# Performance work log

Measured on AMD Instinct MI355X. Metric: run time of the kernel, lower is better.

Reference implementation:

```python
import jax, jax.numpy as jnp
import numpy as np

B, N, D = 256, 512, 64  # batch, positions, channels; units = spatial_units = D


def setup_inputs() -> dict:
    key = jax.random.key(0)
    ks = jax.random.split(key, 9)
    g = 1.0 / np.sqrt(D)  # glorot-ish scale for square matrices
    return {
        "x": jax.random.normal(ks[0], (B, N, D), dtype=jnp.float32),
        "Wq_t": jax.random.normal(ks[1], (D, D), dtype=jnp.float32) * g,
        "Wk_t": jax.random.normal(ks[2], (D, D), dtype=jnp.float32) * g,
        "Wv_t": jax.random.normal(ks[3], (D, D), dtype=jnp.float32) * g,
        "Wq_s": jax.random.normal(ks[4], (D, D), dtype=jnp.float32) * g,
        "Wk_s": jax.random.normal(ks[5], (D, D), dtype=jnp.float32) * g,
        "Wv_s": jax.random.normal(ks[6], (D, D), dtype=jnp.float32) * g,
        "Wd_t": jax.random.normal(ks[7], (D, D), dtype=jnp.float32) * g,
        "bd_t": jnp.zeros((D,), dtype=jnp.float32),
        "Wd_s": jax.random.normal(ks[8], (D, D), dtype=jnp.float32) * g,
        "bd_s": jnp.zeros((D,), dtype=jnp.float32),
    }


def _branch(x, Wq, Wk, Wv, Wd, bd):
    # x: [B, N, D]; one self-attention branch followed by a Dense layer.
    q = jnp.einsum("bnd,de->bne", x, Wq)
    k = jnp.einsum("bnd,de->bne", x, Wk)
    v = jnp.einsum("bnd,de->bne", x, Wv)
    scale = 1.0 / jnp.sqrt(jnp.asarray(Wk.shape[-1], dtype=x.dtype))
    scores = jnp.einsum("bne,bme->bnm", q, k) * scale  # [B, N, N]
    w = jax.nn.softmax(scores, axis=-1)
    attn = jnp.einsum("bnm,bmd->bnd", w, v)
    return jnp.einsum("bnd,de->bne", attn, Wd) + bd


def reference(x, Wq_t, Wk_t, Wv_t, Wq_s, Wk_s, Wv_s, Wd_t, bd_t, Wd_s, bd_s):
    temporal = _branch(x, Wq_t, Wk_t, Wv_t, Wd_t, bd_t)
    spatial = _branch(x, Wq_s, Wk_s, Wv_s, Wd_s, bd_s)
    gate = jax.nn.sigmoid(temporal + spatial)
    return x * gate
```

## Files before the change

### kernel.cpp

```cpp
#include <hip/hip_runtime.h>

typedef __attribute__((ext_vector_type(8))) short short8;
typedef __attribute__((ext_vector_type(4))) short short4v;
typedef __attribute__((ext_vector_type(4))) float float4v;

#define MFMA16(a, b, c) __builtin_amdgcn_mfma_f32_16x16x32_bf16((a), (b), (c), 0, 0, 0)

constexpr int kN = 512;
constexpr int kD = 64;
constexpr int kThreads = 1024;

constexpr int LDS_TOTAL_BYTES = 79872 * 2;

static __device__ __forceinline__ unsigned short f2bf(float f) {
  unsigned int u = __float_as_uint(f);
  u = (u + 0x7fffu + ((u >> 16) & 1u)) >> 16;
  return (unsigned short)u;
}

__global__ __launch_bounds__(kThreads, 4) void ts_attn_fused(
    const float* __restrict__ x, const float* __restrict__ Wq_t,
    const float* __restrict__ Wk_t, const float* __restrict__ Wv_t,
    const float* __restrict__ Wq_s, const float* __restrict__ Wk_s,
    const float* __restrict__ Wv_s, const float* __restrict__ Wd_t,
    const float* __restrict__ bd_t, const float* __restrict__ Wd_s,
    const float* __restrict__ bd_s, float* __restrict__ out,
    unsigned short* __restrict__ qws) {
  extern __shared__ __align__(16) unsigned short smem_us[];
  unsigned short* Ksw = smem_us;
  unsigned short* Vsw = smem_us + 32768;
  unsigned short* Wdsw = smem_us + 65536;
  unsigned short* rep = smem_us + 69632;

  const int tid = threadIdx.x;
  const int wv = tid >> 6;
  const int lane = tid & 63;
  const int ln = lane & 15;
  const int quad = lane >> 4;
  const int b = blockIdx.x;

  const float* xb = x + (size_t)b * (kN * kD);
  float* outb = out + (size_t)b * (kN * kD);
  unsigned short* qb = qws + (size_t)b * (kN * kD);

  const int sd = tid >> 4;
  const int se0 = (tid & 15) * 4;
  const int sbase = (sd >> 3) * 512 + (sd & 7);

  float bdsum[4];
#pragma unroll
  for (int nt = 0; nt < 4; ++nt) bdsum[nt] = bd_t[nt * 16 + ln] + bd_s[nt * 16 + ln];

  float4v acc_t[2][4];

#pragma unroll 1
  for (int br = 0; br < 2; ++br) {
    const float* Wq = br ? Wq_s : Wq_t;
    const float* Wk = br ? Wk_s : Wk_t;
    const float* Wv = br ? Wv_s : Wv_t;
    const float* Wd = br ? Wd_s : Wd_t;

    {
      const float* srcs[3] = {Wq, Wk, Wv};
      unsigned short* dsts[3] = {rep, rep + 4096, Wdsw};
#pragma unroll
      for (int g = 0; g < 3; ++g) {
        const float4v u = *reinterpret_cast<const float4v*>(srcs[g] + sd * 64 + se0);
        unsigned short* dst = dsts[g];
#pragma unroll
        for (int i = 0; i < 4; ++i) dst[sbase + (se0 + i) * 8] = f2bf(u[i]);
      }
    }
    __syncthreads();

#pragma unroll 1
    for (int mi = 0; mi < 2; ++mi) {
      const int mt = wv + mi * 16;
      const int mrow = mt * 16 + ln;
      short8 xa0, xa1;
      {
        const float4v* p0 = reinterpret_cast<const float4v*>(xb + mrow * 64 + quad * 8);
        const float4v u0 = p0[0], v0 = p0[1];
        const float4v* p1 = reinterpret_cast<const float4v*>(xb + mrow * 64 + 32 + quad * 8);
        const float4v u1 = p1[0], v1 = p1[1];
#pragma unroll
        for (int i = 0; i < 4; ++i) {
          xa0[i] = (short)f2bf(u0[i]);
          xa0[4 + i] = (short)f2bf(v0[i]);
          xa1[i] = (short)f2bf(u1[i]);
          xa1[4 + i] = (short)f2bf(v1[i]);
        }
      }
#pragma unroll
      for (int g = 0; g < 3; ++g) {
        const unsigned short* Wl = (g == 0) ? rep : (g == 1) ? (rep + 4096) : Wdsw;
#pragma unroll
        for (int nt = 0; nt < 4; ++nt) {
          const short8 b0 = *reinterpret_cast<const short8*>(Wl + quad * 512 + (nt * 16 + ln) * 8);
          const short8 b1 = *reinterpret_cast<const short8*>(Wl + (4 + quad) * 512 + (nt * 16 + ln) * 8);
          float4v acc = {0.f, 0.f, 0.f, 0.f};
          acc = MFMA16(xa0, b0, acc);
          acc = MFMA16(xa1, b1, acc);
          if (g == 0) {
            const int ehi = nt * 2 + (ln >> 3);
            const int elo = ln & 7;
#pragma unroll
            for (int r = 0; r < 4; ++r)
              qb[ehi * 4096 + (mt * 16 + quad * 4 + r) * 8 + elo] = f2bf(acc[r]);
          } else if (g == 1) {
            const int ehi = nt * 2 + (ln >> 3);
            const int elo = ln & 7;
#pragma unroll
            for (int r = 0; r < 4; ++r)
              Ksw[ehi * 4096 + (mt * 16 + quad * 4 + r) * 8 + elo] = f2bf(acc[r]);
          } else {
            short4v pk;
#pragma unroll
            for (int r = 0; r < 4; ++r) pk[r] = (short)f2bf(acc[r]);
            const int vbase =
                (mt * 2 + (quad >> 1)) * 512 + (nt * 16 + ln) * 8 + (quad & 1) * 4;
            *reinterpret_cast<short4v*>(Vsw + vbase) = pk;
          }
        }
      }
    }
    __syncthreads();

    {
      const float4v u = *reinterpret_cast<const float4v*>(Wd + sd * 64 + se0);
#pragma unroll
      for (int i = 0; i < 4; ++i) Wdsw[sbase + (se0 + i) * 8] = f2bf(u[i]);
    }
    __syncthreads();

    unsigned short* buf = rep + wv * 640;
#pragma unroll 1
    for (int qi = 0; qi < 2; ++qi) {
      const int qt = wv + qi * 16;
      const short8 q0 = *reinterpret_cast<const short8*>(qb + quad * 4096 + (qt * 16 + ln) * 8);
      const short8 q1 = *reinterpret_cast<const short8*>(qb + (4 + quad) * 4096 + (qt * 16 + ln) * 8);

      float sum[4] = {0.f, 0.f, 0.f, 0.f};
      float4v o[4];
#pragma unroll
      for (int i = 0; i < 4; ++i) o[i] = (float4v){0.f, 0.f, 0.f, 0.f};

#pragma unroll 2
      for (int kc = 0; kc < 16; ++kc) {
#pragma unroll
        for (int t2 = 0; t2 < 2; ++t2) {
          const int nt = kc * 2 + t2;
          const short8 k0 = *reinterpret_cast<const short8*>(Ksw + quad * 4096 + (nt * 16 + ln) * 8);
          const short8 k1 =
              *reinterpret_cast<const short8*>(Ksw + (4 + quad) * 4096 + (nt * 16 + ln) * 8);
          float4v acc = {0.f, 0.f, 0.f, 0.f};
          acc = MFMA16(q0, k0, acc);
          acc = MFMA16(q1, k1, acc);
#pragma unroll
          for (int r = 0; r < 4; ++r) {
            const float p = __expf(acc[r] * 0.125f);
            sum[r] += p;
            buf[(quad * 4 + r) * 40 + t2 * 16 + ln] = f2bf(p);
          }
        }
        asm volatile("s_waitcnt lgkmcnt(0)" ::: "memory");
        const short8 pa = *reinterpret_cast<const short8*>(buf + ln * 40 + quad * 8);
#pragma unroll
        for (int nto = 0; nto < 4; ++nto) {
          const short8 vf =
              *reinterpret_cast<const short8*>(Vsw + (kc * 4 + quad) * 512 + (nto * 16 + ln) * 8);
          o[nto] = MFMA16(pa, vf, o[nto]);
        }
        asm volatile("s_waitcnt lgkmcnt(0)" ::: "memory");
      }

#pragma unroll
      for (int dd = 1; dd < 16; dd <<= 1)
#pragma unroll
        for (int r = 0; r < 4; ++r) sum[r] += __shfl_xor(sum[r], dd, 64);
      float inv[4];
#pragma unroll
      for (int r = 0; r < 4; ++r) inv[r] = 1.0f / sum[r];

#pragma unroll
      for (int nto = 0; nto < 2; ++nto)
#pragma unroll
        for (int r = 0; r < 4; ++r)
          buf[(quad * 4 + r) * 40 + nto * 16 + ln] = f2bf(o[nto][r] * inv[r]);
      asm volatile("s_waitcnt lgkmcnt(0)" ::: "memory");
      const short8 a0 = *reinterpret_cast<const short8*>(buf + ln * 40 + quad * 8);
      asm volatile("s_waitcnt lgkmcnt(0)" ::: "memory");
#pragma unroll
      for (int nto = 2; nto < 4; ++nto)
#pragma unroll
        for (int r = 0; r < 4; ++r)
          buf[(quad * 4 + r) * 40 + (nto - 2) * 16 + ln] = f2bf(o[nto][r] * inv[r]);
      asm volatile("s_waitcnt lgkmcnt(0)" ::: "memory");
      const short8 a1 = *reinterpret_cast<const short8*>(buf + ln * 40 + quad * 8);

#pragma unroll
      for (int nt = 0; nt < 4; ++nt) {
        const short8 w0 = *reinterpret_cast<const short8*>(Wdsw + quad * 512 + (nt * 16 + ln) * 8);
        const short8 w1 = *reinterpret_cast<const short8*>(Wdsw + (4 + quad) * 512 + (nt * 16 + ln) * 8);
        float4v d4 = {0.f, 0.f, 0.f, 0.f};
        d4 = MFMA16(a0, w0, d4);
        d4 = MFMA16(a1, w1, d4);
        if (br == 0) {
          acc_t[qi][nt] = d4;
        } else {
          const int m0 = qt * 16 + quad * 4;
          const int col = nt * 16 + ln;
#pragma unroll
          for (int r = 0; r < 4; ++r) {
            const float z = acc_t[qi][nt][r] + d4[r] + bdsum[nt];
            const float gate = 1.0f / (1.0f + __expf(-z));
            outb[(m0 + r) * 64 + col] = xb[(m0 + r) * 64 + col] * gate;
          }
        }
      }
    }
    __syncthreads();
  }
}

extern "C" void kernel_launch(void* const* d_in, const int* in_sizes, int n_in,
                              void* d_out, int out_size, void* d_ws, size_t ws_size,
                              hipStream_t stream) {
  const float* x = (const float*)d_in[0];
  const float* Wq_t = (const float*)d_in[1];
  const float* Wk_t = (const float*)d_in[2];
  const float* Wv_t = (const float*)d_in[3];
  const float* Wq_s = (const float*)d_in[4];
  const float* Wk_s = (const float*)d_in[5];
  const float* Wv_s = (const float*)d_in[6];
  const float* Wd_t = (const float*)d_in[7];
  const float* bd_t = (const float*)d_in[8];
  const float* Wd_s = (const float*)d_in[9];
  const float* bd_s = (const float*)d_in[10];
  float* out = (float*)d_out;
  unsigned short* qws = (unsigned short*)d_ws;

  hipFuncSetAttribute(reinterpret_cast<const void*>(ts_attn_fused),
                      hipFuncAttributeMaxDynamicSharedMemorySize, LDS_TOTAL_BYTES);
  ts_attn_fused<<<dim3(256), dim3(kThreads), LDS_TOTAL_BYTES, stream>>>(
      x, Wq_t, Wk_t, Wv_t, Wq_s, Wk_s, Wv_s, Wd_t, bd_t, Wd_s, bd_s, out, qws);
}
```

Baseline: 208.7 us.

## Keep Q in registers, batch score MFMAs, spill temporal branch result to output

Q is now kept in registers and transposed through the per-wave LDS scratch buffer, so it no longer makes a round trip through a global workspace. The score loop computes eight S tiles back to back before the softmax and PV phase, which reduces the s_waitcnt stalls between MFMA groups. The temporal branch result is written to the output buffer and read back in the spatial branch, replacing the acc_t registers. This frees registers at the cost of an extra global write and read per element.

Result: no change. 205.6 us (-1.5%).

```diff
diff --git a/kernel.cpp b/kernel.cpp
--- a/kernel.cpp
+++ b/kernel.cpp
@@ -24,8 +24,7 @@
     const float* __restrict__ Wq_s, const float* __restrict__ Wk_s,
     const float* __restrict__ Wv_s, const float* __restrict__ Wd_t,
     const float* __restrict__ bd_t, const float* __restrict__ Wd_s,
-    const float* __restrict__ bd_s, float* __restrict__ out,
-    unsigned short* __restrict__ qws) {
+    const float* __restrict__ bd_s, float* __restrict__ out) {
   extern __shared__ __align__(16) unsigned short smem_us[];
   unsigned short* Ksw = smem_us;
   unsigned short* Vsw = smem_us + 32768;
@@ -41,7 +40,6 @@
 
   const float* xb = x + (size_t)b * (kN * kD);
   float* outb = out + (size_t)b * (kN * kD);
-  unsigned short* qb = qws + (size_t)b * (kN * kD);
 
   const int sd = tid >> 4;
   const int se0 = (tid & 15) * 4;
@@ -50,8 +48,6 @@
   float bdsum[4];
 #pragma unroll
   for (int nt = 0; nt < 4; ++nt) bdsum[nt] = bd_t[nt * 16 + ln] + bd_s[nt * 16 + ln];
-
-  float4v acc_t[2][4];
 
 #pragma unroll 1
   for (int br = 0; br < 2; ++br) {
@@ -73,6 +69,7 @@
     }
     __syncthreads();
 
+    short4v qd[2][4];
 #pragma unroll 1
     for (int mi = 0; mi < 2; ++mi) {
       const int mt = wv + mi * 16;
@@ -97,16 +94,16 @@
 #pragma unroll
         for (int nt = 0; nt < 4; ++nt) {
           const short8 b0 = *reinterpret_cast<const short8*>(Wl + quad * 512 + (nt * 16 + ln) * 8);
-          const short8 b1 = *reinterpret_cast<const short8*>(Wl + (4 + quad) * 512 + (nt * 16 + ln) * 8);
+          const short8 b1 =
+              *reinterpret_cast<const short8*>(Wl + (4 + quad) * 512 + (nt * 16 + ln) * 8);
           float4v acc = {0.f, 0.f, 0.f, 0.f};
           acc = MFMA16(xa0, b0, acc);
           acc = MFMA16(xa1, b1, acc);
           if (g == 0) {
-            const int ehi = nt * 2 + (ln >> 3);
-            const int elo = ln & 7;
-#pragma unroll
-            for (int r = 0; r < 4; ++r)
-              qb[ehi * 4096 + (mt * 16 + quad * 4 + r) * 8 + elo] = f2bf(acc[r]);
+            short4v pk;
+#pragma unroll
+            for (int r = 0; r < 4; ++r) pk[r] = (short)f2bf(acc[r]);
+            qd[mi][nt] = pk;
           } else if (g == 1) {
             const int ehi = nt * 2 + (ln >> 3);
             const int elo = ln & 7;
@@ -117,8 +114,7 @@
             short4v pk;
 #pragma unroll
             for (int r = 0; r < 4; ++r) pk[r] = (short)f2bf(acc[r]);
-            const int vbase =
-                (mt * 2 + (quad >> 1)) * 512 + (nt * 16 + ln) * 8 + (quad & 1) * 4;
+            const int vbase = (mt * 2 + (quad >> 1)) * 512 + (nt * 16 + ln) * 8 + (quad & 1) * 4;
             *reinterpret_cast<short4v*>(Vsw + vbase) = pk;
           }
         }
@@ -137,41 +133,65 @@
 #pragma unroll 1
     for (int qi = 0; qi < 2; ++qi) {
       const int qt = wv + qi * 16;
-      const short8 q0 = *reinterpret_cast<const short8*>(qb + quad * 4096 + (qt * 16 + ln) * 8);
-      const short8 q1 = *reinterpret_cast<const short8*>(qb + (4 + quad) * 4096 + (qt * 16 + ln) * 8);
+
+      short8 q0, q1;
+#pragma unroll
+      for (int nt = 0; nt < 2; ++nt)
+#pragma unroll
+        for (int r = 0; r < 4; ++r)
+          buf[(quad * 4 + r) * 40 + nt * 16 + ln] = (unsigned short)qd[qi][nt][r];
+      asm volatile("s_waitcnt lgkmcnt(0)" ::: "memory");
+      q0 = *reinterpret_cast<const short8*>(buf + ln * 40 + quad * 8);
+#pragma unroll
+      for (int nt = 2; nt < 4; ++nt)
+#pragma unroll
+        for (int r = 0; r < 4; ++r)
+          buf[(quad * 4 + r) * 40 + (nt - 2) * 16 + ln] = (unsigned short)qd[qi][nt][r];
+      asm volatile("s_waitcnt lgkmcnt(0)" ::: "memory");
+      q1 = *reinterpret_cast<const short8*>(buf + ln * 40 + quad * 8);
 
       float sum[4] = {0.f, 0.f, 0.f, 0.f};
       float4v o[4];
 #pragma unroll
       for (int i = 0; i < 4; ++i) o[i] = (float4v){0.f, 0.f, 0.f, 0.f};
 
-#pragma unroll 2
-      for (int kc = 0; kc < 16; ++kc) {
-#pragma unroll
-        for (int t2 = 0; t2 < 2; ++t2) {
-          const int nt = kc * 2 + t2;
-          const short8 k0 = *reinterpret_cast<const short8*>(Ksw + quad * 4096 + (nt * 16 + ln) * 8);
+#pragma unroll 1
+      for (int sc = 0; sc < 4; ++sc) {
+        float4v s[8];
+#pragma unroll
+        for (int t = 0; t < 8; ++t) {
+          const int nt = sc * 8 + t;
+          const short8 k0 =
+              *reinterpret_cast<const short8*>(Ksw + quad * 4096 + (nt * 16 + ln) * 8);
           const short8 k1 =
               *reinterpret_cast<const short8*>(Ksw + (4 + quad) * 4096 + (nt * 16 + ln) * 8);
           float4v acc = {0.f, 0.f, 0.f, 0.f};
           acc = MFMA16(q0, k0, acc);
           acc = MFMA16(q1, k1, acc);
-#pragma unroll
-          for (int r = 0; r < 4; ++r) {
-            const float p = __expf(acc[r] * 0.125f);
-            sum[r] += p;
-            buf[(quad * 4 + r) * 40 + t2 * 16 + ln] = f2bf(p);
-          }
-        }
-        asm volatile("s_waitcnt lgkmcnt(0)" ::: "memory");
-        const short8 pa = *reinterpret_cast<const short8*>(buf + ln * 40 + quad * 8);
-#pragma unroll
-        for (int nto = 0; nto < 4; ++nto) {
-          const short8 vf =
-              *reinterpret_cast<const short8*>(Vsw + (kc * 4 + quad) * 512 + (nto * 16 + ln) * 8);
-          o[nto] = MFMA16(pa, vf, o[nto]);
-        }
-        asm volatile("s_waitcnt lgkmcnt(0)" ::: "memory");
+          s[t] = acc;
+        }
+#pragma unroll
+        for (int kc2 = 0; kc2 < 4; ++kc2) {
+          const int kcg = sc * 4 + kc2;
+#pragma unroll
+          for (int t2 = 0; t2 < 2; ++t2) {
+            const float4v sv = s[kc2 * 2 + t2];
+#pragma unroll
+            for (int r = 0; r < 4; ++r) {
+              const float p = __expf(sv[r] * 0.125f);
+              sum[r] += p;
+              buf[(quad * 4 + r) * 40 + t2 * 16 + ln] = f2bf(p);
+            }
+          }
+          asm volatile("s_waitcnt lgkmcnt(0)" ::: "memory");
+          const short8 pa = *reinterpret_cast<const short8*>(buf + ln * 40 + quad * 8);
+#pragma unroll
+          for (int nto = 0; nto < 4; ++nto) {
+            const short8 vf =
+                *reinterpret_cast<const short8*>(Vsw + (kcg * 4 + quad) * 512 + (nto * 16 + ln) * 8);
+            o[nto] = MFMA16(pa, vf, o[nto]);
+          }
+        }
       }
 
 #pragma unroll
@@ -189,7 +209,6 @@
           buf[(quad * 4 + r) * 40 + nto * 16 + ln] = f2bf(o[nto][r] * inv[r]);
       asm volatile("s_waitcnt lgkmcnt(0)" ::: "memory");
       const short8 a0 = *reinterpret_cast<const short8*>(buf + ln * 40 + quad * 8);
-      asm volatile("s_waitcnt lgkmcnt(0)" ::: "memory");
 #pragma unroll
       for (int nto = 2; nto < 4; ++nto)
 #pragma unroll
@@ -201,18 +220,20 @@
 #pragma unroll
       for (int nt = 0; nt < 4; ++nt) {
         const short8 w0 = *reinterpret_cast<const short8*>(Wdsw + quad * 512 + (nt * 16 + ln) * 8);
-        const short8 w1 = *reinterpret_cast<const short8*>(Wdsw + (4 + quad) * 512 + (nt * 16 + ln) * 8);
+        const short8 w1 =
+            *reinterpret_cast<const short8*>(Wdsw + (4 + quad) * 512 + (nt * 16 + ln) * 8);
         float4v d4 = {0.f, 0.f, 0.f, 0.f};
         d4 = MFMA16(a0, w0, d4);
         d4 = MFMA16(a1, w1, d4);
+        const int m0 = qt * 16 + quad * 4;
+        const int col = nt * 16 + ln;
         if (br == 0) {
-          acc_t[qi][nt] = d4;
+#pragma unroll
+          for (int r = 0; r < 4; ++r) outb[(m0 + r) * 64 + col] = d4[r];
         } else {
-          const int m0 = qt * 16 + quad * 4;
-          const int col = nt * 16 + ln;
 #pragma unroll
           for (int r = 0; r < 4; ++r) {
-            const float z = acc_t[qi][nt][r] + d4[r] + bdsum[nt];
+            const float z = outb[(m0 + r) * 64 + col] + d4[r] + bdsum[nt];
             const float gate = 1.0f / (1.0f + __expf(-z));
             outb[(m0 + r) * 64 + col] = xb[(m0 + r) * 64 + col] * gate;
           }
@@ -238,10 +259,9 @@
   const float* Wd_s = (const float*)d_in[9];
   const float* bd_s = (const float*)d_in[10];
   float* out = (float*)d_out;
-  unsigned short* qws = (unsigned short*)d_ws;
 
   hipFuncSetAttribute(reinterpret_cast<const void*>(ts_attn_fused),
                       hipFuncAttributeMaxDynamicSharedMemorySize, LDS_TOTAL_BYTES);
   ts_attn_fused<<<dim3(256), dim3(kThreads), LDS_TOTAL_BYTES, stream>>>(
-      x, Wq_t, Wk_t, Wv_t, Wq_s, Wk_s, Wv_s, Wd_t, bd_t, Wd_s, bd_s, out, qws);
+      x, Wq_t, Wk_t, Wv_t, Wq_s, Wk_s, Wv_s, Wd_t, bd_t, Wd_s, bd_s, out);
 }
```
